# Performance work log

Hardware: AMD Instinct MI355X
Metric: run time of the kernel (lower is better)

## Reference

```python
import jax, jax.numpy as jnp
import numpy as np

N = 50000          # nodes
E = 800000         # edges
H = 160            # hidden_dim = 32*5
HC = 32            # hidden_dim // 5 per-feature encoder width
LM = 768           # lm_input_dim
NUM_REL = 2
LEAK = 0.01        # nn.LeakyReLU default negative_slope


def leaky_relu(v):
    return jnp.where(v >= 0, v, LEAK * v)


def setup_inputs() -> dict:
    key = jax.random.key(0)
    ks = jax.random.split(key, 32)

    def lin(k, din, dout):
        kw, _ = jax.random.split(k)
        s = 1.0 / np.sqrt(din)
        W = jax.random.uniform(kw, (din, dout), jnp.float32, -s, s)
        b = jnp.zeros((dout,), jnp.float32)
        return W, b

    inp = {}
    inp["pre_x"] = jax.random.normal(ks[0], (N, LM), jnp.float32)
    inp["x"] = jnp.zeros((N, H), jnp.float32)  # dead input (overwritten in forward)
    inp["edge_index"] = jax.random.randint(ks[1], (2, E), 0, N, jnp.int32)
    inp["edge_type"] = jax.random.randint(ks[2], (E,), 0, NUM_REL, jnp.int32)
    inp["num_prop"] = jax.random.normal(ks[3], (N, 6), jnp.float32)
    inp["num_category"] = jax.random.normal(ks[4], (N, 11), jnp.float32)
    inp["des_tensor"] = jax.random.normal(ks[5], (N, LM), jnp.float32)
    inp["tweet_tensor"] = jax.random.normal(ks[6], (N, LM), jnp.float32)

    inp["W_np"], inp["b_np"] = lin(ks[7], 6, HC)
    inp["W_nc"], inp["b_nc"] = lin(ks[8], 11, HC)
    inp["W_des"], inp["b_des"] = lin(ks[9], LM, HC)
    inp["W_text"], inp["b_text"] = lin(ks[10], LM, HC)
    inp["W_tweet"], inp["b_tweet"] = lin(ks[11], LM, HC)
    inp["W_in"], inp["b_in"] = lin(ks[12], H, H)

    s = 1.0 / np.sqrt(H)
    inp["W_rel1"] = jax.random.uniform(ks[13], (NUM_REL, H, H), jnp.float32, -s, s)
    inp["W_root1"], inp["b_conv1"] = lin(ks[14], H, H)
    inp["W_rel2"] = jax.random.uniform(ks[15], (NUM_REL, H, H), jnp.float32, -s, s)
    inp["W_root2"], inp["b_conv2"] = lin(ks[16], H, H)

    inp["W_o1"], inp["b_o1"] = lin(ks[17], H, 80)
    inp["W_o2"], inp["b_o2"] = lin(ks[18], 80, 2)
    return inp


def rgcn_conv(h, src, dst, edge_type, W_rel, W_root, b):
    # PyG RGCNConv: per-relation mean aggregation + root transform + bias.
    out = h @ W_root + b
    for r in range(NUM_REL):
        w = (edge_type == r).astype(h.dtype)              # [E]
        msg = (h @ W_rel[r])[src] * w[:, None]            # [E, H] gather of transformed feats
        summed = jax.ops.segment_sum(msg, dst, num_segments=N)
        cnt = jax.ops.segment_sum(w, dst, num_segments=N)
        out = out + summed / jnp.maximum(cnt, 1.0)[:, None]
    return out


def reference(pre_x, x, edge_index, edge_type, num_prop, num_category, des_tensor,
              tweet_tensor, W_np, b_np, W_nc, b_nc, W_des, b_des, W_text, b_text,
              W_tweet, b_tweet, W_in, b_in, W_rel1, W_root1, b_conv1,
              W_rel2, W_root2, b_conv2, W_o1, b_o1, W_o2, b_o2):
    # Dropout is identity at inference.
    n = leaky_relu(num_prop @ W_np + b_np)
    c = leaky_relu(num_category @ W_nc + b_nc)
    d = leaky_relu(des_tensor @ W_des + b_des)
    tw = leaky_relu(tweet_tensor @ W_text + b_text)
    pre_t = leaky_relu(pre_x @ W_tweet + b_tweet)
    h = jnp.concatenate((n, c, d, tw, pre_t), axis=1)     # [N, 160]
    h = leaky_relu(h @ W_in + b_in)

    src, dst = edge_index[0], edge_index[1]
    h = rgcn_conv(h, src, dst, edge_type, W_rel1, W_root1, b_conv1)
    h = rgcn_conv(h, src, dst, edge_type, W_rel2, W_root2, b_conv2)

    em = leaky_relu(h @ W_o1 + b_o1)                      # [N, 80]
    out = em @ W_o2 + b_o2                                # [N, 2]
    return out, em
```

## Files before the change

### kernel.cpp

```cpp
#include <hip/hip_runtime.h>

#define NN 50000
#define EE 800000
#define HH 160
#define LMD 768
#define NBLK 196
#define GB64 782

typedef __attribute__((ext_vector_type(8))) short s8;
typedef __attribute__((ext_vector_type(4))) float f4;

__device__ __forceinline__ float lrelu(float v){ return v >= 0.f ? v : 0.01f*v; }

__device__ __forceinline__ short f2b(float f){
  unsigned int u = __float_as_uint(f);
  unsigned int r = (u + 0x7fffu + ((u >> 16) & 1u)) >> 16;
  return (short)r;
}
__device__ __forceinline__ float b2f(short s){
  return __uint_as_float(((unsigned int)(unsigned short)s) << 16);
}

struct WD { const float* s; short* d; int K; int C; int ldd; };
struct WDs { WD w[11]; int* cnt2; };
__global__ __launch_bounds__(256) void wt_k(WDs ds)
{
  if (blockIdx.y == 11) {
    int idx = blockIdx.x*256 + threadIdx.x;
    #pragma unroll
    for (int j = 0; j < 4; ++j) {
      int i = idx + j*25600;
      if (i < 2*NN) ds.cnt2[i] = 0;
    }
    return;
  }
  WD w = ds.w[blockIdx.y];
  int idx = blockIdx.x*256 + threadIdx.x;
  if (idx < w.K * w.C) {
    int k = idx / w.C, c = idx - k*w.C;
    w.d[(size_t)c*w.ldd + k] = f2b(w.s[idx]);
  }
}

__global__ __launch_bounds__(256) void enc_small_k(
    const float* __restrict__ npx, const float* __restrict__ ncx,
    const float* __restrict__ Wnp, const float* __restrict__ bnp,
    const float* __restrict__ Wnc, const float* __restrict__ bnc,
    short* __restrict__ out)
{
  int gid = blockIdx.x*256 + threadIdx.x;
  int row = gid >> 6, c = gid & 63;
  if (row >= NN) return;
  float acc;
  if (c < 32) {
    acc = bnp[c];
    #pragma unroll
    for (int k = 0; k < 6; ++k) acc += npx[row*6+k]*Wnp[k*32+c];
  } else {
    int cc = c - 32;
    acc = bnc[cc];
    #pragma unroll
    for (int k = 0; k < 11; ++k) acc += ncx[row*11+k]*Wnc[k*32+cc];
  }
  out[(size_t)row*HH + c] = f2b(lrelu(acc));
}

template<int C, bool XBF>
__device__ __forceinline__ void gemm_body(
    const void* __restrict__ Xv, int ldx,
    const short* __restrict__ WT, const float* __restrict__ bias,
    short* __restrict__ outb, int ldo, int K, int leaky, int r0)
{
  constexpr int NT = C/16;
  constexpr int NW = (C*4 + 255)/256;
  __shared__ __attribute__((aligned(16))) short Xs[64*40];
  __shared__ __attribute__((aligned(16))) short Ws[C*40];
  const int t = threadIdx.x;
  const int w = t >> 6, L = t & 63;
  const int lm = L & 15, lq = L >> 4;
  const int srow = t >> 2, skg = t & 3;
  const int gr = r0 + srow;

  f4 acc[NT];
  #pragma unroll
  for (int j = 0; j < NT; ++j) acc[j] = (f4){0.f,0.f,0.f,0.f};

  s8 xv = (s8){0,0,0,0,0,0,0,0};
  s8 wv[NW];

  if (gr < NN) {
    if (XBF) {
      xv = *(const s8*)((const short*)Xv + (size_t)gr*ldx + skg*8);
    } else {
      const float* xp = (const float*)Xv + (size_t)gr*ldx + skg*8;
      float4 a = *(const float4*)xp, b = *(const float4*)(xp+4);
      xv[0]=f2b(a.x); xv[1]=f2b(a.y); xv[2]=f2b(a.z); xv[3]=f2b(a.w);
      xv[4]=f2b(b.x); xv[5]=f2b(b.y); xv[6]=f2b(b.z); xv[7]=f2b(b.w);
    }
  }
  #pragma unroll
  for (int s = 0; s < NW; ++s) {
    int i = t + s*256;
    if (i < C*4) { int c = i>>2, kg = i&3; wv[s] = *(const s8*)(WT + (size_t)c*K + kg*8); }
  }

  for (int k0 = 0; k0 < K; k0 += 32) {
    if (k0) __syncthreads();
    *(s8*)&Xs[srow*40 + skg*8] = xv;
    #pragma unroll
    for (int s = 0; s < NW; ++s) {
      int i = t + s*256;
      if (i < C*4) { int c = i>>2, kg = i&3; *(s8*)&Ws[c*40 + kg*8] = wv[s]; }
    }
    __syncthreads();
    int kn = k0 + 32;
    if (kn < K) {
      if (gr < NN) {
        if (XBF) {
          xv = *(const s8*)((const short*)Xv + (size_t)gr*ldx + kn + skg*8);
        } else {
          const float* xp = (const float*)Xv + (size_t)gr*ldx + kn + skg*8;
          float4 a = *(const float4*)xp, b = *(const float4*)(xp+4);
          xv[0]=f2b(a.x); xv[1]=f2b(a.y); xv[2]=f2b(a.z); xv[3]=f2b(a.w);
          xv[4]=f2b(b.x); xv[5]=f2b(b.y); xv[6]=f2b(b.z); xv[7]=f2b(b.w);
        }
      }
      #pragma unroll
      for (int s = 0; s < NW; ++s) {
        int i = t + s*256;
        if (i < C*4) { int c = i>>2, kg = i&3; wv[s] = *(const s8*)(WT + (size_t)c*K + kn + kg*8); }
      }
    }
    s8 a = *(const s8*)&Xs[(w*16 + lm)*40 + lq*8];
    #pragma unroll
    for (int j = 0; j < NT; ++j) {
      s8 bf = *(const s8*)&Ws[(j*16 + lm)*40 + lq*8];
      acc[j] = __builtin_amdgcn_mfma_f32_16x16x32_bf16(a, bf, acc[j], 0, 0, 0);
    }
  }

  #pragma unroll
  for (int j = 0; j < NT; ++j) {
    int col = j*16 + lm;
    float bv = bias ? bias[col] : 0.f;
    #pragma unroll
    for (int r = 0; r < 4; ++r) {
      int go = r0 + w*16 + lq*4 + r;
      if (go < NN) {
        float v = acc[j][r] + bv;
        if (leaky) v = lrelu(v);
        outb[(size_t)go*ldo + col] = f2b(v);
      }
    }
  }
}

struct Enc3 { const float* X[3]; const short* WT[3]; const float* B[3]; short* out[3]; };
__global__ __launch_bounds__(256) void enc3_k(Enc3 e)
{
  int j = blockIdx.y;
  gemm_body<32,false>(e.X[j], LMD, e.WT[j], e.B[j], e.out[j], HH, LMD, 1, blockIdx.x*64);
}

__global__ __launch_bounds__(256) void dgemm_k(
    const short* __restrict__ X, int ldx,
    const short* __restrict__ WT, const float* __restrict__ bias,
    short* __restrict__ outb, int ldo, int K, int leaky)
{
  gemm_body<160,true>(X, ldx, WT, bias, outb, ldo, K, leaky, blockIdx.x*64);
}

__global__ __launch_bounds__(256) void head_k(
    const short* __restrict__ X,
    const short* __restrict__ WT, const float* __restrict__ bias,
    const float* __restrict__ W2, const float* __restrict__ b2,
    float* __restrict__ em, float* __restrict__ out)
{
  constexpr int C = 80, NT = 5;
  __shared__ __attribute__((aligned(16))) short Xs[128*40];
  __shared__ __attribute__((aligned(16))) short Ws[C*40];
  __shared__ float emS[128][81];
  const int t = threadIdx.x;
  const int r0 = blockIdx.x*128;
  const int w = t >> 6, L = t & 63;
  const int lm = L & 15, lq = L >> 4;

  f4 acc[2][NT];
  #pragma unroll
  for (int i = 0; i < 2; ++i)
    #pragma unroll
    for (int j = 0; j < NT; ++j) acc[i][j] = (f4){0.f,0.f,0.f,0.f};

  for (int k0 = 0; k0 < HH; k0 += 32) {
    for (int i = t; i < 512; i += 256) {
      int row = i >> 2, kg = i & 3;
      int gr = r0 + row;
      s8 v = (s8){0,0,0,0,0,0,0,0};
      if (gr < NN) v = *(const s8*)(X + (size_t)gr*HH + k0 + kg*8);
      *(s8*)&Xs[row*40 + kg*8] = v;
    }
    for (int i = t; i < C*4; i += 256) {
      int c = i >> 2, kg = i & 3;
      *(s8*)&Ws[c*40 + kg*8] = *(const s8*)(WT + (size_t)c*HH + k0 + kg*8);
    }
    __syncthreads();
    s8 a0 = *(const s8*)&Xs[(w*32 + lm)*40 + lq*8];
    s8 a1 = *(const s8*)&Xs[(w*32 + 16 + lm)*40 + lq*8];
    #pragma unroll
    for (int j = 0; j < NT; ++j) {
      s8 bf = *(const s8*)&Ws[(j*16 + lm)*40 + lq*8];
      acc[0][j] = __builtin_amdgcn_mfma_f32_16x16x32_bf16(a0, bf, acc[0][j], 0, 0, 0);
      acc[1][j] = __builtin_amdgcn_mfma_f32_16x16x32_bf16(a1, bf, acc[1][j], 0, 0, 0);
    }
    __syncthreads();
  }

  #pragma unroll
  for (int i = 0; i < 2; ++i) {
    #pragma unroll
    for (int j = 0; j < NT; ++j) {
      int col = j*16 + lm;
      float bv = bias[col];
      #pragma unroll
      for (int r = 0; r < 4; ++r) {
        int lr = w*32 + i*16 + lq*4 + r;
        int gr = r0 + lr;
        if (gr < NN) {
          float v = lrelu(acc[i][j][r] + bv);
          em[(size_t)gr*80 + col] = v;
          emS[lr][col] = v;
        }
      }
    }
  }
  __syncthreads();
  if (t < 128) {
    int gr = r0 + t;
    if (gr < NN) {
      float a0 = b2[0], a1 = b2[1];
      #pragma unroll
      for (int k = 0; k < 80; ++k) {
        float v = emS[t][k];
        a0 += v*W2[k*2]; a1 += v*W2[k*2+1];
      }
      out[gr*2] = a0; out[gr*2+1] = a1;
    }
  }
}

__global__ __launch_bounds__(256) void hist_k(
    const int* __restrict__ dst, const int* __restrict__ et, int* __restrict__ cnt2)
{
  int e = blockIdx.x*256 + threadIdx.x;
  if (e < EE) atomicAdd(&cnt2[et[e]*NN + dst[e]], 1);
}

__global__ __launch_bounds__(256) void scan1_k(
    const int* __restrict__ cnt2, float* __restrict__ inv2,
    int* __restrict__ off1, int* __restrict__ partials)
{
  __shared__ int sh[256];
  int t = threadIdx.x;
  int i = blockIdx.x*256 + t;
  int c0 = 0, c1 = 0;
  if (i < NN) {
    c0 = cnt2[i]; c1 = cnt2[NN + i];
    inv2[i]      = 1.f / (float)max(c0, 1);
    inv2[NN + i] = 1.f / (float)max(c1, 1);
  }
  sh[t] = c0 + c1;
  __syncthreads();
  for (int s = 1; s < 256; s <<= 1) {
    int add = (t >= s) ? sh[t-s] : 0;
    __syncthreads();
    sh[t] += add;
    __syncthreads();
  }
  if (i < NN) off1[i] = sh[t];
  if (t == 255) partials[blockIdx.x] = sh[255];
}

__global__ __launch_bounds__(256) void scan2_k(int* __restrict__ partials)
{
  __shared__ int sh[256];
  int t = threadIdx.x;
  sh[t] = (t < NBLK) ? partials[t] : 0;
  __syncthreads();
  for (int s = 1; s < 256; s <<= 1) {
    int add = (t >= s) ? sh[t-s] : 0;
    __syncthreads();
    sh[t] += add;
    __syncthreads();
  }
  if (t < NBLK) partials[t] = (t == 0) ? 0 : sh[t-1];
}

__global__ __launch_bounds__(256) void scan3_k(
    int* __restrict__ off, int* __restrict__ cursor, const int* __restrict__ partials)
{
  int i = blockIdx.x*256 + threadIdx.x;
  if (i < NN) {
    int v = off[i+1] + partials[i >> 8];
    off[i+1] = v;
    if (i + 1 < NN) cursor[i+1] = v;
  }
  if (i == 0) { off[0] = 0; cursor[0] = 0; }
}

__global__ __launch_bounds__(256) void scatter_k(
    const int* __restrict__ src, const int* __restrict__ dst, const int* __restrict__ et,
    int* __restrict__ cursor, int* __restrict__ elist)
{
  int e = blockIdx.x*256 + threadIdx.x;
  if (e >= EE) return;
  int d = dst[e];
  int pos = atomicAdd(&cursor[d], 1);
  elist[pos] = (src[e] << 1) | et[e];
}

__global__ __launch_bounds__(256) void aggregate_k(
    const int* __restrict__ off, const int* __restrict__ elist,
    const float* __restrict__ inv2, short* __restrict__ X)
{
  int gid = blockIdx.x*256 + threadIdx.x;
  int d = gid / 20, q = gid - d*20;
  if (d >= NN) return;
  int beg = off[d], end = off[d+1];
  float a0[8], a1[8];
  #pragma unroll
  for (int i = 0; i < 8; ++i) { a0[i] = 0.f; a1[i] = 0.f; }
  int p = beg;
  for (; p + 2 <= end; p += 2) {
    int pk0 = elist[p], pk1 = elist[p+1];
    s8 v0 = *(const s8*)(X + (size_t)(pk0 >> 1)*480 + q*8);
    s8 v1 = *(const s8*)(X + (size_t)(pk1 >> 1)*480 + q*8);
    float m10 = (float)(pk0 & 1), m00 = 1.f - m10;
    float m11 = (float)(pk1 & 1), m01 = 1.f - m11;
    #pragma unroll
    for (int i = 0; i < 8; ++i) {
      float f0 = b2f(v0[i]), f1 = b2f(v1[i]);
      a0[i] += f0*m00 + f1*m01;
      a1[i] += f0*m10 + f1*m11;
    }
  }
  if (p < end) {
    int pk = elist[p];
    s8 v = *(const s8*)(X + (size_t)(pk >> 1)*480 + q*8);
    float m1 = (float)(pk & 1), m0 = 1.f - m1;
    #pragma unroll
    for (int i = 0; i < 8; ++i) {
      float f = b2f(v[i]);
      a0[i] += f*m0; a1[i] += f*m1;
    }
  }
  float i0 = inv2[d], i1 = inv2[NN + d];
  s8 o0, o1;
  #pragma unroll
  for (int i = 0; i < 8; ++i) { o0[i] = f2b(a0[i]*i0); o1[i] = f2b(a1[i]*i1); }
  *(s8*)(X + (size_t)d*480 + 160 + q*8) = o0;
  *(s8*)(X + (size_t)d*480 + 320 + q*8) = o1;
}

extern "C" void kernel_launch(void* const* d_in, const int* in_sizes, int n_in,
                              void* d_out, int out_size, void* d_ws, size_t ws_size,
                              hipStream_t stream)
{
  const float* pre_x   = (const float*)d_in[0];
  const int*   eidx    = (const int*)d_in[2];
  const int*   etype   = (const int*)d_in[3];
  const float* num_prop= (const float*)d_in[4];
  const float* num_cat = (const float*)d_in[5];
  const float* des     = (const float*)d_in[6];
  const float* tweet   = (const float*)d_in[7];
  const float* W_np=(const float*)d_in[8],  *b_np=(const float*)d_in[9];
  const float* W_nc=(const float*)d_in[10], *b_nc=(const float*)d_in[11];
  const float* W_des=(const float*)d_in[12],*b_des=(const float*)d_in[13];
  const float* W_text=(const float*)d_in[14],*b_text=(const float*)d_in[15];
  const float* W_tweet=(const float*)d_in[16],*b_tweet=(const float*)d_in[17];
  const float* W_in=(const float*)d_in[18], *b_in=(const float*)d_in[19];
  const float* W_rel1=(const float*)d_in[20], *W_root1=(const float*)d_in[21], *b_c1=(const float*)d_in[22];
  const float* W_rel2=(const float*)d_in[23], *W_root2=(const float*)d_in[24], *b_c2=(const float*)d_in[25];
  const float* W_o1=(const float*)d_in[26], *b_o1=(const float*)d_in[27];
  const float* W_o2=(const float*)d_in[28], *b_o2=(const float*)d_in[29];

  float* out = (float*)d_out;
  float* em  = out + (size_t)NN*2;

  short* Acat = (short*)d_ws;
  short* X1   = Acat + (size_t)NN*HH;
  short* X2   = X1   + (size_t)NN*480;
  short* WT   = X2   + (size_t)NN*480;
  short* WT_des   = WT;
  short* WT_text  = WT +  24576;
  short* WT_tweet = WT +  49152;
  short* WT_in    = WT +  73728;
  short* WT_cat1  = WT +  99328;
  short* WT_cat2  = WT + 176128;
  short* WT_o1    = WT + 252928;

  int*   cnt2    = (int*)(WT + 265728);
  float* inv2    = (float*)(cnt2 + 2*NN);
  int*   off     = (int*)(inv2 + 2*NN);
  int*   partials= off + NN + 1;
  int*   cursor  = partials + 256;
  int*   elist   = cursor + NN;

  const int* src = eidx;
  const int* dst = eidx + EE;

  WDs ds;
  ds.w[0]  = (WD){W_des,          WT_des,         LMD, 32, LMD};
  ds.w[1]  = (WD){W_text,         WT_text,        LMD, 32, LMD};
  ds.w[2]  = (WD){W_tweet,        WT_tweet,       LMD, 32, LMD};
  ds.w[3]  = (WD){W_in,           WT_in,          HH, HH, HH};
  ds.w[4]  = (WD){W_root1,        WT_cat1,        HH, HH, 480};
  ds.w[5]  = (WD){W_rel1,         WT_cat1 + 160,  HH, HH, 480};
  ds.w[6]  = (WD){W_rel1 + HH*HH, WT_cat1 + 320,  HH, HH, 480};
  ds.w[7]  = (WD){W_root2,        WT_cat2,        HH, HH, 480};
  ds.w[8]  = (WD){W_rel2,         WT_cat2 + 160,  HH, HH, 480};
  ds.w[9]  = (WD){W_rel2 + HH*HH, WT_cat2 + 320,  HH, HH, 480};
  ds.w[10] = (WD){W_o1,           WT_o1,          HH, 80, HH};
  ds.cnt2  = cnt2;
  wt_k<<<dim3(100, 12), 256, 0, stream>>>(ds);

  hist_k  <<<(EE+255)/256, 256, 0, stream>>>(dst, etype, cnt2);
  scan1_k <<<NBLK, 256, 0, stream>>>(cnt2, inv2, off+1, partials);
  scan2_k <<<1,    256, 0, stream>>>(partials);
  scan3_k <<<NBLK, 256, 0, stream>>>(off, cursor, partials);
  scatter_k<<<(EE+255)/256, 256, 0, stream>>>(src, dst, etype, cursor, elist);

  enc_small_k<<<(NN*64+255)/256, 256, 0, stream>>>(num_prop, num_cat, W_np,b_np, W_nc,b_nc, Acat);
  Enc3 e3;
  e3.X[0]=des;     e3.WT[0]=WT_des;   e3.B[0]=b_des;   e3.out[0]=Acat+64;
  e3.X[1]=tweet;   e3.WT[1]=WT_text;  e3.B[1]=b_text;  e3.out[1]=Acat+96;
  e3.X[2]=pre_x;   e3.WT[2]=WT_tweet; e3.B[2]=b_tweet; e3.out[2]=Acat+128;
  enc3_k<<<dim3(GB64, 3), 256, 0, stream>>>(e3);

  dgemm_k<<<GB64,256,0,stream>>>(Acat, HH, WT_in, b_in, X1, 480, HH, 1);

  aggregate_k<<<(NN*20+255)/256, 256, 0, stream>>>(off, elist, inv2, X1);
  dgemm_k<<<GB64,256,0,stream>>>(X1, 480, WT_cat1, b_c1, X2, 480, 480, 0);

  aggregate_k<<<(NN*20+255)/256, 256, 0, stream>>>(off, elist, inv2, X2);
  dgemm_k<<<GB64,256,0,stream>>>(X2, 480, WT_cat2, b_c2, Acat, HH, 480, 0);

  head_k<<<(NN+127)/128,256,0,stream>>>(Acat, WT_o1, b_o1, W_o2, b_o2, em, out);
}
```

Measured before the change: 819.2 us.

## Replace LDS-staged GEMM with per-wave direct-load MFMA tiles

The shared GEMM body no longer stages X and W tiles through LDS with block-wide barriers. Each wave now owns a 16-row tile, loads its A fragments straight from global memory with one-step register prefetch, and reads B fragments directly from the transposed weights. This removes the LDS copies and __syncthreads, at the cost of every wave re-reading the weight matrix from global memory/L2 rather than sharing one staged copy per block. The grid is resized to four tiles per block and the row bounds checks are dropped, which relies on N being a multiple of 16.

```diff
diff --git a/kernel.cpp b/kernel.cpp
--- a/kernel.cpp
+++ b/kernel.cpp
@@ -5,7 +5,7 @@
 #define HH 160
 #define LMD 768
 #define NBLK 196
-#define GB64 782
+#define NTILE 3125
 
 typedef __attribute__((ext_vector_type(8))) short s8;
 typedef __attribute__((ext_vector_type(4))) float f4;
@@ -66,91 +66,62 @@
 }
 
 template<int C, bool XBF>
-__device__ __forceinline__ void gemm_body(
+__device__ __forceinline__ void dmfma_body(
     const void* __restrict__ Xv, int ldx,
     const short* __restrict__ WT, const float* __restrict__ bias,
-    short* __restrict__ outb, int ldo, int K, int leaky, int r0)
+    short* __restrict__ outb, int ldo, int K, int leaky, int tile)
 {
   constexpr int NT = C/16;
-  constexpr int NW = (C*4 + 255)/256;
-  __shared__ __attribute__((aligned(16))) short Xs[64*40];
-  __shared__ __attribute__((aligned(16))) short Ws[C*40];
-  const int t = threadIdx.x;
-  const int w = t >> 6, L = t & 63;
+  const int L = threadIdx.x & 63;
   const int lm = L & 15, lq = L >> 4;
-  const int srow = t >> 2, skg = t & 3;
-  const int gr = r0 + srow;
+  const int gr = tile*16 + lm;
 
   f4 acc[NT];
   #pragma unroll
   for (int j = 0; j < NT; ++j) acc[j] = (f4){0.f,0.f,0.f,0.f};
 
-  s8 xv = (s8){0,0,0,0,0,0,0,0};
-  s8 wv[NW];
-
-  if (gr < NN) {
+  const short* xb = XBF ? ((const short*)Xv + (size_t)gr*ldx + lq*8) : nullptr;
+  const float* xf = XBF ? nullptr : ((const float*)Xv + (size_t)gr*ldx + lq*8);
+
+  auto load_a = [&](int k0) -> s8 {
     if (XBF) {
-      xv = *(const s8*)((const short*)Xv + (size_t)gr*ldx + skg*8);
+      return *(const s8*)(xb + k0);
     } else {
-      const float* xp = (const float*)Xv + (size_t)gr*ldx + skg*8;
-      float4 a = *(const float4*)xp, b = *(const float4*)(xp+4);
-      xv[0]=f2b(a.x); xv[1]=f2b(a.y); xv[2]=f2b(a.z); xv[3]=f2b(a.w);
-      xv[4]=f2b(b.x); xv[5]=f2b(b.y); xv[6]=f2b(b.z); xv[7]=f2b(b.w);
-    }
-  }
-  #pragma unroll
-  for (int s = 0; s < NW; ++s) {
-    int i = t + s*256;
-    if (i < C*4) { int c = i>>2, kg = i&3; wv[s] = *(const s8*)(WT + (size_t)c*K + kg*8); }
-  }
-
+      float4 a = *(const float4*)(xf + k0);
+      float4 b = *(const float4*)(xf + k0 + 4);
+      s8 v;
+      v[0]=f2b(a.x); v[1]=f2b(a.y); v[2]=f2b(a.z); v[3]=f2b(a.w);
+      v[4]=f2b(b.x); v[5]=f2b(b.y); v[6]=f2b(b.z); v[7]=f2b(b.w);
+      return v;
+    }
+  };
+
+  const short* wb = WT + (size_t)lm*K + lq*8;
+
+  s8 aN = load_a(0);
   for (int k0 = 0; k0 < K; k0 += 32) {
-    if (k0) __syncthreads();
-    *(s8*)&Xs[srow*40 + skg*8] = xv;
-    #pragma unroll
-    for (int s = 0; s < NW; ++s) {
-      int i = t + s*256;
-      if (i < C*4) { int c = i>>2, kg = i&3; *(s8*)&Ws[c*40 + kg*8] = wv[s]; }
-    }
-    __syncthreads();
+    s8 aC = aN;
     int kn = k0 + 32;
-    if (kn < K) {
-      if (gr < NN) {
-        if (XBF) {
-          xv = *(const s8*)((const short*)Xv + (size_t)gr*ldx + kn + skg*8);
-        } else {
-          const float* xp = (const float*)Xv + (size_t)gr*ldx + kn + skg*8;
-          float4 a = *(const float4*)xp, b = *(const float4*)(xp+4);
-          xv[0]=f2b(a.x); xv[1]=f2b(a.y); xv[2]=f2b(a.z); xv[3]=f2b(a.w);
-          xv[4]=f2b(b.x); xv[5]=f2b(b.y); xv[6]=f2b(b.z); xv[7]=f2b(b.w);
-        }
-      }
-      #pragma unroll
-      for (int s = 0; s < NW; ++s) {
-        int i = t + s*256;
-        if (i < C*4) { int c = i>>2, kg = i&3; wv[s] = *(const s8*)(WT + (size_t)c*K + kn + kg*8); }
-      }
-    }
-    s8 a = *(const s8*)&Xs[(w*16 + lm)*40 + lq*8];
-    #pragma unroll
-    for (int j = 0; j < NT; ++j) {
-      s8 bf = *(const s8*)&Ws[(j*16 + lm)*40 + lq*8];
-      acc[j] = __builtin_amdgcn_mfma_f32_16x16x32_bf16(a, bf, acc[j], 0, 0, 0);
-    }
+    if (kn < K) aN = load_a(kn);
+    s8 bv[NT];
+    #pragma unroll
+    for (int j = 0; j < NT; ++j)
+      bv[j] = *(const s8*)(wb + (size_t)j*16*K + k0);
+    #pragma unroll
+    for (int j = 0; j < NT; ++j)
+      acc[j] = __builtin_amdgcn_mfma_f32_16x16x32_bf16(aC, bv[j], acc[j], 0, 0, 0);
   }
 
   #pragma unroll
   for (int j = 0; j < NT; ++j) {
     int col = j*16 + lm;
-    float bv = bias ? bias[col] : 0.f;
+    float bvv = bias ? bias[col] : 0.f;
     #pragma unroll
     for (int r = 0; r < 4; ++r) {
-      int go = r0 + w*16 + lq*4 + r;
-      if (go < NN) {
-        float v = acc[j][r] + bv;
-        if (leaky) v = lrelu(v);
-        outb[(size_t)go*ldo + col] = f2b(v);
-      }
+      int go = tile*16 + lq*4 + r;
+      float v = acc[j][r] + bvv;
+      if (leaky) v = lrelu(v);
+      outb[(size_t)go*ldo + col] = f2b(v);
     }
   }
 }
@@ -158,8 +129,10 @@
 struct Enc3 { const float* X[3]; const short* WT[3]; const float* B[3]; short* out[3]; };
 __global__ __launch_bounds__(256) void enc3_k(Enc3 e)
 {
+  int tile = blockIdx.x*4 + (threadIdx.x >> 6);
+  if (tile >= NTILE) return;
   int j = blockIdx.y;
-  gemm_body<32,false>(e.X[j], LMD, e.WT[j], e.B[j], e.out[j], HH, LMD, 1, blockIdx.x*64);
+  dmfma_body<32,false>(e.X[j], LMD, e.WT[j], e.B[j], e.out[j], HH, LMD, 1, tile);
 }
 
 __global__ __launch_bounds__(256) void dgemm_k(
@@ -167,7 +140,9 @@
     const short* __restrict__ WT, const float* __restrict__ bias,
     short* __restrict__ outb, int ldo, int K, int leaky)
 {
-  gemm_body<160,true>(X, ldx, WT, bias, outb, ldo, K, leaky, blockIdx.x*64);
+  int tile = blockIdx.x*4 + (threadIdx.x >> 6);
+  if (tile >= NTILE) return;
+  dmfma_body<160,true>(X, ldx, WT, bias, outb, ldo, K, leaky, tile);
 }
 
 __global__ __launch_bounds__(256) void head_k(
@@ -434,15 +409,16 @@
   e3.X[0]=des;     e3.WT[0]=WT_des;   e3.B[0]=b_des;   e3.out[0]=Acat+64;
   e3.X[1]=tweet;   e3.WT[1]=WT_text;  e3.B[1]=b_text;  e3.out[1]=Acat+96;
   e3.X[2]=pre_x;   e3.WT[2]=WT_tweet; e3.B[2]=b_tweet; e3.out[2]=Acat+128;
-  enc3_k<<<dim3(GB64, 3), 256, 0, stream>>>(e3);
-
-  dgemm_k<<<GB64,256,0,stream>>>(Acat, HH, WT_in, b_in, X1, 480, HH, 1);
+  const int GW = (NTILE + 3) / 4;
+  enc3_k<<<dim3(GW, 3), 256, 0, stream>>>(e3);
+
+  dgemm_k<<<GW,256,0,stream>>>(Acat, HH, WT_in, b_in, X1, 480, HH, 1);
 
   aggregate_k<<<(NN*20+255)/256, 256, 0, stream>>>(off, elist, inv2, X1);
-  dgemm_k<<<GB64,256,0,stream>>>(X1, 480, WT_cat1, b_c1, X2, 480, 480, 0);
+  dgemm_k<<<GW,256,0,stream>>>(X1, 480, WT_cat1, b_c1, X2, 480, 480, 0);
 
   aggregate_k<<<(NN*20+255)/256, 256, 0, stream>>>(off, elist, inv2, X2);
-  dgemm_k<<<GB64,256,0,stream>>>(X2, 480, WT_cat2, b_c2, Acat, HH, 480, 0);
+  dgemm_k<<<GW,256,0,stream>>>(X2, 480, WT_cat2, b_c2, Acat, HH, 480, 0);
 
   head_k<<<(NN+127)/128,256,0,stream>>>(Acat, WT_o1, b_o1, W_o2, b_o2, em, out);
 }
```

Result: slower. 862.6 us (+5.3%).
